# Optimization experiments

Measured on AMD Instinct MI355X. Metric: run time of the kernel, lower is better.

The kernel has to match this reference:

```python
import jax, jax.numpy as jnp
import numpy as np
from jax import lax

B, L, D, H = 48, 512, 384, 384


def setup_inputs() -> dict:
    key = jax.random.key(0)
    ks = jax.random.split(key, 8)
    def w(k, shape, fan):
        return jax.random.normal(k, shape, jnp.float32) / np.float32(np.sqrt(fan))
    return {
        "v": jax.random.normal(ks[0], (B, L, D), jnp.float32),
        "mask": jnp.ones((B, L), jnp.bool_),
        "Wp_cur": w(ks[1], (D, H), D),      # torch Wp (applied to v_i)
        "Wp_seq": w(ks[2], (D, H), D),      # torch Wp_ (applied to all of v)
        "V": w(ks[3], (H,), H),             # torch V: Linear(H, 1, bias=False)
        "W_ih": w(ks[4], (3 * H, 2 * D), 2 * D),  # GRUCell input weights
        "W_hh": w(ks[5], (3 * H, H), H),           # GRUCell hidden weights
        "b_ih": jnp.zeros((3 * H,), jnp.float32),
        "b_hh": jnp.zeros((3 * H,), jnp.float32),
    }


def _forward(v, mask, Wp_cur, Wp_seq, V, W_ih, W_hh, b_ih, b_hh):
    Bv, Lv, _ = v.shape
    Hh = W_hh.shape[1]
    # Torch recomputes Wp_(v) identically every step; hoist it (same math).
    Wpv = jnp.einsum('bld,dh->blh', v, Wp_seq)            # [B,L,H]
    neg = jnp.where(mask, 0.0, -1e30).astype(v.dtype)     # additive attention mask [B,L]

    def step(h, vi):                                       # vi: [B,D], h: [B,H]
        wpi = vi @ Wp_cur                                  # [B,H]
        x = jnp.tanh(Wpv + wpi[:, None, :])                # [B,L,H]
        s = jnp.einsum('blh,h->bl', x, V) + neg            # scores [B,L]
        a = jax.nn.softmax(s, axis=1)                      # masked softmax
        c = jnp.einsum('bl,bld->bd', a, v)                 # context [B,D]
        r = jnp.concatenate([vi, c], axis=1)               # [B,2D]
        gi = r @ W_ih.T + b_ih
        gh = h @ W_hh.T + b_hh
        ir, iz, inn = jnp.split(gi, 3, axis=1)
        hr, hz, hn = jnp.split(gh, 3, axis=1)
        rg = jax.nn.sigmoid(ir + hr)
        zg = jax.nn.sigmoid(iz + hz)
        ng = jnp.tanh(inn + rg * hn)
        hnew = (1.0 - zg) * ng + zg * h                    # PyTorch GRUCell update
        return hnew, hnew

    h0 = jnp.zeros((Bv, Hh), v.dtype)
    h_last, hs = lax.scan(jax.checkpoint(step), h0, jnp.swapaxes(v, 0, 1))
    hs = jnp.swapaxes(hs, 0, 1)                            # [B,L,H]
    # dropout p=0.0 -> identity; h = hs[:, -1]
    return hs, h_last


def reference(v, mask, Wp_cur, Wp_seq, V, W_ih, W_hh, b_ih, b_hh):
    return _forward(v, mask, Wp_cur, Wp_seq, V, W_ih, W_hh, b_ih, b_hh)
```

## Files before the change

### kernel.cpp

```cpp
#include <hip/hip_runtime.h>


typedef unsigned short u16;
typedef unsigned int u32;
typedef short short8 __attribute__((ext_vector_type(8)));
typedef float f32x4 __attribute__((ext_vector_type(4)));
typedef float f4 __attribute__((ext_vector_type(4)));
typedef _Float16 h2_t __attribute__((ext_vector_type(2)));
typedef _Float16 h8_t __attribute__((ext_vector_type(8)));

#define BDIM 48
#define LDIM 512
#define DDIM 384
#define HDIM 384

__device__ __forceinline__ float bf2f(u16 u) { return __uint_as_float(((u32)u) << 16); }
__device__ __forceinline__ u16 f2bf(float f) {
  u32 x = __float_as_uint(f);
  u32 r = (x + 0x7fffu + ((x >> 16) & 1u)) >> 16;
  return (u16)r;
}
__device__ __forceinline__ float sigm(float x) {
  return __builtin_amdgcn_rcpf(1.f + exp2f(-1.4426950408889634f * x));
}
__device__ __forceinline__ float tanh_f(float x) {
  float e = exp2f(2.885390081777927f * x);
  return 1.f - 2.f * __builtin_amdgcn_rcpf(e + 1.f);
}

__device__ __forceinline__ void load16(const void* src, long ld, int isf32,
                                       long row, int kbase, short8& o0, short8& o1)
{
  if (isf32) {
    const float* s = (const float*)src + row * ld + kbase;
    f4 q0 = *(const f4*)(s);
    f4 q1 = *(const f4*)(s + 4);
    f4 q2 = *(const f4*)(s + 8);
    f4 q3 = *(const f4*)(s + 12);
    short8 a, b;
    a[0] = (short)f2bf(q0[0]); a[1] = (short)f2bf(q0[1]);
    a[2] = (short)f2bf(q0[2]); a[3] = (short)f2bf(q0[3]);
    a[4] = (short)f2bf(q1[0]); a[5] = (short)f2bf(q1[1]);
    a[6] = (short)f2bf(q1[2]); a[7] = (short)f2bf(q1[3]);
    b[0] = (short)f2bf(q2[0]); b[1] = (short)f2bf(q2[1]);
    b[2] = (short)f2bf(q2[2]); b[3] = (short)f2bf(q2[3]);
    b[4] = (short)f2bf(q3[0]); b[5] = (short)f2bf(q3[1]);
    b[6] = (short)f2bf(q3[2]); b[7] = (short)f2bf(q3[3]);
    o0 = a; o1 = b;
  } else {
    const u16* s = (const u16*)src + row * ld + kbase;
    o0 = *(const short8*)s;
    o1 = *(const short8*)(s + 8);
  }
}

__global__ __launch_bounds__(256) void gemm_bt(
    const void* __restrict__ A1, const void* __restrict__ A2,
    long lda1, long lda2, int ksplit, int a1f, int a2f,
    const void* __restrict__ Bm, long ldb, int bfm,
    u16* __restrict__ Out, int N, int K,
    long strideA, long strideB, long strideO,
    const float* __restrict__ bias, int epi_exp2, int out_bf16)
{
  __shared__ u16 As[128][40];
  __shared__ u16 Bs[128][40];
  const int tid = threadIdx.x;
  const int lane = tid & 63;
  const int w = tid >> 6;
  const int wm = w >> 1, wn = w & 1;
  const int l15 = lane & 15, quad = lane >> 4;
  const long m0 = (long)blockIdx.x * 128;
  const long n0 = (long)blockIdx.y * 128;
  const int z = blockIdx.z;
  const char* A1p = (const char*)A1 + (long)z * strideA * (a1f ? 4 : 2);
  const char* A2p = (const char*)A2 + (long)z * strideA * (a2f ? 4 : 2);
  const char* Bp  = (const char*)Bm + (long)z * strideB * (bfm ? 4 : 2);
  u16* Op = Out + (long)z * strideO;

  const int r2 = tid & 127;
  const int half = tid >> 7;

  f32x4 acc[4][4];
#pragma unroll
  for (int a = 0; a < 4; a++)
#pragma unroll
    for (int c = 0; c < 4; c++) acc[a][c] = (f32x4){0.f, 0.f, 0.f, 0.f};

  for (int k0 = 0; k0 < K; k0 += 32) {
    const void* srcA; long lda; int kk; int af;
    if (k0 < ksplit) { srcA = A1p; lda = lda1; kk = k0; af = a1f; }
    else             { srcA = A2p; lda = lda2; kk = k0 - ksplit; af = a2f; }
    short8 a0, a1, b0, b1;
    load16(srcA, lda, af, m0 + r2, kk + half * 16, a0, a1);
    load16(Bp, ldb, bfm, n0 + r2, k0 + half * 16, b0, b1);
    __syncthreads();
    *(short8*)&As[r2][half * 16] = a0;
    *(short8*)&As[r2][half * 16 + 8] = a1;
    *(short8*)&Bs[r2][half * 16] = b0;
    *(short8*)&Bs[r2][half * 16 + 8] = b1;
    __syncthreads();
    short8 af_[4], bf_[4];
#pragma unroll
    for (int mt = 0; mt < 4; mt++) af_[mt] = *(const short8*)&As[wm * 64 + mt * 16 + l15][quad * 8];
#pragma unroll
    for (int nt = 0; nt < 4; nt++) bf_[nt] = *(const short8*)&Bs[wn * 64 + nt * 16 + l15][quad * 8];
#pragma unroll
    for (int mt = 0; mt < 4; mt++)
#pragma unroll
      for (int nt = 0; nt < 4; nt++)
        acc[mt][nt] = __builtin_amdgcn_mfma_f32_16x16x32_bf16(af_[mt], bf_[nt], acc[mt][nt], 0, 0, 0);
  }

#pragma unroll
  for (int mt = 0; mt < 4; mt++) {
#pragma unroll
    for (int nt = 0; nt < 4; nt++) {
      const long col = n0 + wn * 64 + nt * 16 + l15;
      float bv = bias ? bias[col] : 0.f;
#pragma unroll
      for (int rg = 0; rg < 4; rg++) {
        long row = m0 + wm * 64 + mt * 16 + quad * 4 + rg;
        float vv = acc[mt][nt][rg] + bv;
        if (epi_exp2) {
          float t = vv * 2.885390081777927f;
          t = fminf(fmaxf(t, -15.9f), 15.9f);
          vv = exp2f(t);
        }
        long idx = row * (long)N + col;
        if (out_bf16) Op[idx] = f2bf(vv);
        else ((_Float16*)Op)[idx] = (_Float16)vv;
      }
    }
  }
}

__global__ void transpose_f2b(const float* __restrict__ src, u16* __restrict__ dst,
                              int rows, int cols, long sstride, long dstride)
{
  __shared__ float t[32][33];
  const int bz = blockIdx.z;
  const float* s = src + (long)bz * sstride;
  u16* d = dst + (long)bz * dstride;
  const int c0 = blockIdx.x * 32, r0 = blockIdx.y * 32;
  const int tx = threadIdx.x, ty = threadIdx.y;
#pragma unroll
  for (int j = 0; j < 4; j++) t[ty + j * 8][tx] = s[(long)(r0 + ty + j * 8) * cols + c0 + tx];
  __syncthreads();
#pragma unroll
  for (int j = 0; j < 4; j++) d[(long)(c0 + ty + j * 8) * rows + r0 + tx] = f2bf(t[tx][ty + j * 8]);
}

__global__ __launch_bounds__(256) void attn_softmax(
    const _Float16* __restrict__ E, const _Float16* __restrict__ F,
    const float* __restrict__ Vw, u16* __restrict__ Aout)
{
  const int blk = blockIdx.x;
  const int x8 = blk & 7;
  const int rest = blk >> 3;
  const int i = rest & 511;
  const int b = x8 + 8 * (rest >> 9);
  const int tid = threadIdx.x;
  const int lane = tid & 63, w = tid >> 6;
  const int r = lane & 15, sub = lane >> 4;
  __shared__ float Tl[512];
  __shared__ float red[8];

  const h8_t* Fr = (const h8_t*)(F + ((long)b * LDIM + i) * HDIM + r * 24);
  h8_t fq0 = Fr[0], fq1 = Fr[1], fq2 = Fr[2];
  float fv[24], vv[24];
#pragma unroll
  for (int j = 0; j < 8; j++) {
    fv[j] = (float)fq0[j]; fv[8 + j] = (float)fq1[j]; fv[16 + j] = (float)fq2[j];
  }
  const float* Vp = Vw + r * 24;
#pragma unroll
  for (int j = 0; j < 24; j++) vv[j] = Vp[j];

  for (int li = 0; li < 32; ++li) {
    const int l = li * 16 + w * 4 + sub;
    const h8_t* Er = (const h8_t*)(E + ((long)b * LDIM + l) * HDIM + r * 24);
    h8_t e0 = Er[0], e1 = Er[1], e2 = Er[2];
    float p = 0.f;
#pragma unroll
    for (int j = 0; j < 8; j++) {
      p += vv[j]      * __builtin_amdgcn_rcpf((float)e0[j] * fv[j]      + 1.f);
      p += vv[8 + j]  * __builtin_amdgcn_rcpf((float)e1[j] * fv[8 + j]  + 1.f);
      p += vv[16 + j] * __builtin_amdgcn_rcpf((float)e2[j] * fv[16 + j] + 1.f);
    }
    p += __shfl_xor(p, 1);
    p += __shfl_xor(p, 2);
    p += __shfl_xor(p, 4);
    p += __shfl_xor(p, 8);
    if (r == 0) Tl[l] = p;
  }
  __syncthreads();

  const float t0 = Tl[tid], t1 = Tl[tid + 256];
  float mn = fminf(t0, t1);
#pragma unroll
  for (int off = 32; off; off >>= 1) mn = fminf(mn, __shfl_xor(mn, off));
  if (lane == 0) red[w] = mn;
  __syncthreads();
  const float mT = fminf(fminf(red[0], red[1]), fminf(red[2], red[3]));
  const float C2 = 2.885390081777927f;
  float p0 = exp2f(C2 * (mT - t0));
  float p1 = exp2f(C2 * (mT - t1));
  float ssum = p0 + p1;
#pragma unroll
  for (int off = 32; off; off >>= 1) ssum += __shfl_xor(ssum, off);
  if (lane == 0) red[4 + w] = ssum;
  __syncthreads();
  const float Z = (red[4] + red[5]) + (red[6] + red[7]);
  const float inv = __builtin_amdgcn_rcpf(Z);
  u16* Ar = Aout + ((long)b * LDIM + i) * LDIM;
  Ar[tid] = f2bf(p0 * inv);
  Ar[tid + 256] = f2bf(p1 * inv);
}

__global__ __launch_bounds__(512, 2) void recurrence(
    const float* __restrict__ Whh, const float* __restrict__ bhh_g,
    const _Float16* __restrict__ GI, u32* __restrict__ hslots,
    float* __restrict__ out)
{
  const int blk = blockIdx.x;
  const int x8 = blk & 7;
  const int s = blk >> 3;
  const int b = x8 + 8 * (s % 6);
  const int g = s / 6;
  const int tid = threadIdx.x;
  const int tx = tid & 15;
  const int ty = tid >> 4;

  __shared__ _Float16 hall[HDIM];
  __shared__ float gh[288];

  h2_t wv[9][12];
  float bh[9];
#pragma unroll
  for (int q = 0; q < 9; q++) {
    int rr = ty * 9 + q;
    int R = (rr / 96) * 384 + g * 96 + (rr % 96);
    const f4* wq = (const f4*)(Whh + (long)R * HDIM + tx * 24);
#pragma unroll
    for (int t6 = 0; t6 < 6; t6++) {
      f4 u = wq[t6];
      wv[q][2 * t6]     = (h2_t){(_Float16)u[0], (_Float16)u[1]};
      wv[q][2 * t6 + 1] = (h2_t){(_Float16)u[2], (_Float16)u[3]};
    }
    bh[q] = (tx == 0) ? bhh_g[R] : 0.f;
  }

  if (tid < HDIM) hall[tid] = (_Float16)0.f;
  __syncthreads();

  const long gi_base = (long)b * LDIM * 1152;
  const int own = tid >> 5;
  (void)own;
  float hprev = 0.f;

  for (int i = 0; i < LDIM; ++i) {
    float gir = 0.f, giz = 0.f, gin = 0.f;
    if (tid < 96) {
      const long gb = gi_base + (long)i * 1152 + g * 96 + tid;
      gir = (float)GI[gb];
      giz = (float)GI[gb + 384];
      gin = (float)GI[gb + 768];
    }

    if (i > 0) {
      if (tid < HDIM && (tid / 96) != g) {
        u32* p = hslots + (long)(i & 1) * (BDIM * HDIM) + (long)b * HDIM + tid;
        u32 val = __hip_atomic_load(p, __ATOMIC_RELAXED, __HIP_MEMORY_SCOPE_AGENT);
        while ((val >> 16) != (u32)i) {
          __builtin_amdgcn_s_sleep(1);
          val = __hip_atomic_load(p, __ATOMIC_RELAXED, __HIP_MEMORY_SCOPE_AGENT);
        }
        union { u16 u; _Float16 h; } cv;
        cv.u = (u16)val;
        hall[tid] = cv.h;
      }
      __syncthreads();
    }

    h2_t hv[12];
#pragma unroll
    for (int p = 0; p < 12; p++) hv[p] = *(const h2_t*)&hall[tx * 24 + 2 * p];
    float ac[9];
#pragma unroll
    for (int q = 0; q < 9; q++) {
      float a = 0.f;
#pragma unroll
      for (int p = 0; p < 12; p++) a = __builtin_amdgcn_fdot2(wv[q][p], hv[p], a, false);
      ac[q] = a;
    }
#pragma unroll
    for (int q = 0; q < 9; q++) {
      float a = ac[q];
      a += __shfl_xor(a, 1);
      a += __shfl_xor(a, 2);
      a += __shfl_xor(a, 4);
      a += __shfl_xor(a, 8);
      if (tx == 0) gh[ty * 9 + q] = a + bh[q];
    }
    __syncthreads();
    if (tid < 96) {
      const int j = g * 96 + tid;
      float hr = gh[tid], hz = gh[96 + tid], hn = gh[192 + tid];
      float rg = sigm(gir + hr);
      float zg = sigm(giz + hz);
      float ng = tanh_f(gin + rg * hn);
      float hnew = (1.f - zg) * ng + zg * hprev;
      hprev = hnew;
      out[((long)b * LDIM + i) * HDIM + j] = hnew;
      if (i == LDIM - 1) out[(long)BDIM * LDIM * HDIM + (long)b * HDIM + j] = hnew;
      union { _Float16 h; u16 u; } cv;
      cv.h = (_Float16)hnew;
      hall[j] = cv.h;
      if (i + 1 < LDIM) {
        u32 val = ((u32)(i + 1) << 16) | (u32)cv.u;
        __hip_atomic_store(
            hslots + (long)((i + 1) & 1) * (BDIM * HDIM) + (long)b * HDIM + j, val,
            __ATOMIC_RELAXED, __HIP_MEMORY_SCOPE_AGENT);
      }
    }
  }
}

extern "C" void kernel_launch(void* const* d_in, const int* in_sizes, int n_in,
                              void* d_out, int out_size, void* d_ws, size_t ws_size,
                              hipStream_t stream)
{
  (void)in_sizes; (void)n_in; (void)out_size; (void)ws_size;
  const float* v      = (const float*)d_in[0];
  const float* Wp_cur = (const float*)d_in[2];
  const float* Wp_seq = (const float*)d_in[3];
  const float* Vw     = (const float*)d_in[4];
  const float* W_ih   = (const float*)d_in[5];
  const float* W_hh   = (const float*)d_in[6];
  const float* b_ih   = (const float*)d_in[7];
  const float* b_hh   = (const float*)d_in[8];
  float* out = (float*)d_out;

  char* ws = (char*)d_ws;
  size_t off = 0;
  auto alloc = [&](size_t bytes) -> char* {
    char* p = ws + off;
    off += (bytes + 255) & ~(size_t)255;
    return p;
  };
  u32* hslots = (u32*)alloc((size_t)2 * 48 * 384 * 4);
  u16* WpSeqT = (u16*)alloc((size_t)384 * 384 * 2);
  u16* WpCurT = (u16*)alloc((size_t)384 * 384 * 2);
  u16* Cbuf   = (u16*)alloc((size_t)24576 * 384 * 2);
  u16* vT     = (u16*)alloc((size_t)48 * 384 * 512 * 2);
  char* region = alloc((size_t)24576 * 384 * 2 * 2 + (size_t)24576 * 512 * 2);
  _Float16* E  = (_Float16*)region;
  _Float16* F  = (_Float16*)(region + (size_t)24576 * 384 * 2);
  u16* Abuf    = (u16*)(region + (size_t)24576 * 384 * 2 * 2);
  _Float16* GI = (_Float16*)region;

  transpose_f2b<<<dim3(12, 12, 1), dim3(32, 8), 0, stream>>>(Wp_seq, WpSeqT, 384, 384, 0, 0);
  transpose_f2b<<<dim3(12, 12, 1), dim3(32, 8), 0, stream>>>(Wp_cur, WpCurT, 384, 384, 0, 0);
  transpose_f2b<<<dim3(12, 16, 48), dim3(32, 8), 0, stream>>>(v, vT, 512, 384,
                                                              (long)512 * 384, (long)384 * 512);

  gemm_bt<<<dim3(192, 3, 1), 256, 0, stream>>>(v, v, 384, 384, 1 << 30, 1, 1,
                                               WpSeqT, 384, 0,
                                               (u16*)E, 384, 384, 0, 0, 0, nullptr, 1, 0);
  gemm_bt<<<dim3(192, 3, 1), 256, 0, stream>>>(v, v, 384, 384, 1 << 30, 1, 1,
                                               WpCurT, 384, 0,
                                               (u16*)F, 384, 384, 0, 0, 0, nullptr, 1, 0);

  attn_softmax<<<dim3(24576), 256, 0, stream>>>(E, F, Vw, Abuf);

  gemm_bt<<<dim3(4, 3, 48), 256, 0, stream>>>(Abuf, Abuf, 512, 512, 1 << 30, 0, 0,
                                              vT, 512, 0,
                                              Cbuf, 384, 512,
                                              (long)512 * 512, (long)384 * 512, (long)512 * 384,
                                              nullptr, 0, 1);

  gemm_bt<<<dim3(192, 9, 1), 256, 0, stream>>>(v, Cbuf, 384, 384, 384, 1, 0,
                                               W_ih, 768, 1,
                                               (u16*)GI, 1152, 768, 0, 0, 0, b_ih, 0, 0);

  void* args[] = {(void*)&W_hh, (void*)&b_hh, (void*)&GI, (void*)&hslots, (void*)&out};
  hipLaunchCooperativeKernel(recurrence, dim3(192), dim3(512), args, 0, stream);
}
```

Measured before the change: 2.358 ms.

## Remove block barriers from GRU recurrence; poll tagged hidden state directly

Reworks the recurrence kernel so each 16-lane group owns three hidden units end-to-end. The group computes all three gate dot products, reduces them with shuffles, and applies the GRU update without shared memory or __syncthreads. Every thread now polls the full tagged hidden vector from global memory with vector loads. A fast-path buffer is written with workgroup scope and read with sc0 loads, and a mirror buffer written with agent scope serves as a fallback after many spins. GI values for the next step are prefetched one iteration ahead. The cost targeted is barrier and LDS round-trip latency per step; the risk is that the workgroup-scope fast path may not be coherent across CUs, so it could spin until the fallback kicks in, and every thread now generates global polling traffic.

```diff
diff --git a/kernel.cpp b/kernel.cpp
--- a/kernel.cpp
+++ b/kernel.cpp
@@ -8,6 +8,7 @@
 typedef float f4 __attribute__((ext_vector_type(4)));
 typedef _Float16 h2_t __attribute__((ext_vector_type(2)));
 typedef _Float16 h8_t __attribute__((ext_vector_type(8)));
+typedef u32 u32x4 __attribute__((ext_vector_type(4)));
 
 #define BDIM 48
 #define LDIM 512
@@ -219,8 +220,8 @@
 
 __global__ __launch_bounds__(512, 2) void recurrence(
     const float* __restrict__ Whh, const float* __restrict__ bhh_g,
-    const _Float16* __restrict__ GI, u32* __restrict__ hslots,
-    float* __restrict__ out)
+    const _Float16* __restrict__ GI, u32* __restrict__ hfast,
+    u32* __restrict__ hmir, float* __restrict__ out)
 {
   const int blk = blockIdx.x;
   const int x8 = blk & 7;
@@ -230,16 +231,13 @@
   const int tid = threadIdx.x;
   const int tx = tid & 15;
   const int ty = tid >> 4;
-
-  __shared__ _Float16 hall[HDIM];
-  __shared__ float gh[288];
+  const int jbase = g * 96 + ty * 3;
 
   h2_t wv[9][12];
   float bh[9];
 #pragma unroll
   for (int q = 0; q < 9; q++) {
-    int rr = ty * 9 + q;
-    int R = (rr / 96) * 384 + g * 96 + (rr % 96);
+    const int R = (q % 3) * 384 + jbase + (q / 3);
     const f4* wq = (const f4*)(Whh + (long)R * HDIM + tx * 24);
 #pragma unroll
     for (int t6 = 0; t6 < 6; t6++) {
@@ -247,80 +245,148 @@
       wv[q][2 * t6]     = (h2_t){(_Float16)u[0], (_Float16)u[1]};
       wv[q][2 * t6 + 1] = (h2_t){(_Float16)u[2], (_Float16)u[3]};
     }
-    bh[q] = (tx == 0) ? bhh_g[R] : 0.f;
-  }
-
-  if (tid < HDIM) hall[tid] = (_Float16)0.f;
-  __syncthreads();
-
-  const long gi_base = (long)b * LDIM * 1152;
-  const int own = tid >> 5;
-  (void)own;
-  float hprev = 0.f;
+    bh[q] = bhh_g[R];
+  }
+
+  float gc[9], gn[9];
+#pragma unroll
+  for (int q = 0; q < 9; q++) gn[q] = 0.f;
+  if (tx == 0) {
+    const _Float16* gp = GI + (long)b * LDIM * 1152 + jbase;
+#pragma unroll
+    for (int q = 0; q < 9; q++) gn[q] = (float)gp[(q % 3) * 384 + (q / 3)];
+  }
+
+  const u32* fb = hfast + (long)b * HDIM + tx * 24;
+  const u32* mb = hmir  + (long)b * HDIM + tx * 24;
+  u32* sf = hfast + (long)b * HDIM + jbase;
+  u32* sm = hmir  + (long)b * HDIM + jbase;
+  const int SLOT = BDIM * HDIM;
+
+  float hp0 = 0.f, hp1 = 0.f, hp2 = 0.f;
+  int mode = 0;
 
   for (int i = 0; i < LDIM; ++i) {
-    float gir = 0.f, giz = 0.f, gin = 0.f;
-    if (tid < 96) {
-      const long gb = gi_base + (long)i * 1152 + g * 96 + tid;
-      gir = (float)GI[gb];
-      giz = (float)GI[gb + 384];
-      gin = (float)GI[gb + 768];
-    }
-
-    if (i > 0) {
-      if (tid < HDIM && (tid / 96) != g) {
-        u32* p = hslots + (long)(i & 1) * (BDIM * HDIM) + (long)b * HDIM + tid;
-        u32 val = __hip_atomic_load(p, __ATOMIC_RELAXED, __HIP_MEMORY_SCOPE_AGENT);
-        while ((val >> 16) != (u32)i) {
-          __builtin_amdgcn_s_sleep(1);
-          val = __hip_atomic_load(p, __ATOMIC_RELAXED, __HIP_MEMORY_SCOPE_AGENT);
+#pragma unroll
+    for (int q = 0; q < 9; q++) gc[q] = gn[q];
+
+    h2_t hv[12];
+    const bool hh = (i > 0);
+    if (hh) {
+      const u32 itag = (u32)i << 16;
+      const int ofs = (i & 1) ? SLOT : 0;
+      const u32* fp = fb + ofs;
+      const u32* mp = mb + ofs;
+      u32x4 q0, q1, q2, q3, q4, q5;
+      int spins = 0;
+      for (;;) {
+        if (mode == 0) {
+          asm volatile(
+              "global_load_dwordx4 %0, %6, off sc0\n\t"
+              "global_load_dwordx4 %1, %6, off offset:16 sc0\n\t"
+              "global_load_dwordx4 %2, %6, off offset:32 sc0\n\t"
+              "global_load_dwordx4 %3, %6, off offset:48 sc0\n\t"
+              "global_load_dwordx4 %4, %6, off offset:64 sc0\n\t"
+              "global_load_dwordx4 %5, %6, off offset:80 sc0"
+              : "=v"(q0), "=v"(q1), "=v"(q2), "=v"(q3), "=v"(q4), "=v"(q5)
+              : "v"(fp));
+        } else {
+          asm volatile(
+              "global_load_dwordx4 %0, %6, off sc0 sc1\n\t"
+              "global_load_dwordx4 %1, %6, off offset:16 sc0 sc1\n\t"
+              "global_load_dwordx4 %2, %6, off offset:32 sc0 sc1\n\t"
+              "global_load_dwordx4 %3, %6, off offset:48 sc0 sc1\n\t"
+              "global_load_dwordx4 %4, %6, off offset:64 sc0 sc1\n\t"
+              "global_load_dwordx4 %5, %6, off offset:80 sc0 sc1"
+              : "=v"(q0), "=v"(q1), "=v"(q2), "=v"(q3), "=v"(q4), "=v"(q5)
+              : "v"(mp));
         }
-        union { u16 u; _Float16 h; } cv;
-        cv.u = (u16)val;
-        hall[tid] = cv.h;
-      }
-      __syncthreads();
-    }
-
-    h2_t hv[12];
-#pragma unroll
-    for (int p = 0; p < 12; p++) hv[p] = *(const h2_t*)&hall[tx * 24 + 2 * p];
+        asm volatile("s_waitcnt vmcnt(0)" ::: "memory");
+        __builtin_amdgcn_sched_barrier(0);
+        u32 bad = 0;
+#pragma unroll
+        for (int k = 0; k < 4; k++) {
+          bad |= q0[k] ^ itag; bad |= q1[k] ^ itag; bad |= q2[k] ^ itag;
+          bad |= q3[k] ^ itag; bad |= q4[k] ^ itag; bad |= q5[k] ^ itag;
+        }
+        if (!(bad >> 16)) break;
+        if (++spins > 200) mode = 1;
+        __builtin_amdgcn_s_sleep(1);
+      }
+#define UNPK(QQ, P0)                                                        \
+      {                                                                     \
+        union { u32 u; h2_t h; } c0_, c1_;                                  \
+        c0_.u = (QQ[0] & 0xffffu) | (QQ[1] << 16);                          \
+        c1_.u = (QQ[2] & 0xffffu) | (QQ[3] << 16);                          \
+        hv[P0] = c0_.h; hv[P0 + 1] = c1_.h;                                 \
+      }
+      UNPK(q0, 0) UNPK(q1, 2) UNPK(q2, 4) UNPK(q3, 6) UNPK(q4, 8) UNPK(q5, 10)
+#undef UNPK
+    }
+
+    if (tx == 0 && i + 1 < LDIM) {
+      const _Float16* gp = GI + ((long)b * LDIM + (i + 1)) * 1152 + jbase;
+#pragma unroll
+      for (int q = 0; q < 9; q++) gn[q] = (float)gp[(q % 3) * 384 + (q / 3)];
+    }
+
     float ac[9];
-#pragma unroll
-    for (int q = 0; q < 9; q++) {
-      float a = 0.f;
-#pragma unroll
-      for (int p = 0; p < 12; p++) a = __builtin_amdgcn_fdot2(wv[q][p], hv[p], a, false);
-      ac[q] = a;
-    }
-#pragma unroll
-    for (int q = 0; q < 9; q++) {
-      float a = ac[q];
-      a += __shfl_xor(a, 1);
-      a += __shfl_xor(a, 2);
-      a += __shfl_xor(a, 4);
-      a += __shfl_xor(a, 8);
-      if (tx == 0) gh[ty * 9 + q] = a + bh[q];
-    }
-    __syncthreads();
-    if (tid < 96) {
-      const int j = g * 96 + tid;
-      float hr = gh[tid], hz = gh[96 + tid], hn = gh[192 + tid];
-      float rg = sigm(gir + hr);
-      float zg = sigm(giz + hz);
-      float ng = tanh_f(gin + rg * hn);
-      float hnew = (1.f - zg) * ng + zg * hprev;
-      hprev = hnew;
-      out[((long)b * LDIM + i) * HDIM + j] = hnew;
-      if (i == LDIM - 1) out[(long)BDIM * LDIM * HDIM + (long)b * HDIM + j] = hnew;
-      union { _Float16 h; u16 u; } cv;
-      cv.h = (_Float16)hnew;
-      hall[j] = cv.h;
+    if (hh) {
+#pragma unroll
+      for (int q = 0; q < 9; q++) {
+        float a = 0.f;
+#pragma unroll
+        for (int p = 0; p < 12; p++) a = __builtin_amdgcn_fdot2(wv[q][p], hv[p], a, false);
+        a += __shfl_xor(a, 1);
+        a += __shfl_xor(a, 2);
+        a += __shfl_xor(a, 4);
+        a += __shfl_xor(a, 8);
+        ac[q] = a;
+      }
+    } else {
+#pragma unroll
+      for (int q = 0; q < 9; q++) ac[q] = 0.f;
+    }
+
+    if (tx == 0) {
+      float h0n, h1n, h2n;
+      {
+        float rg = sigm(gc[0] + ac[0] + bh[0]);
+        float zg = sigm(gc[1] + ac[1] + bh[1]);
+        float ng = tanh_f(gc[2] + rg * (ac[2] + bh[2]));
+        h0n = (1.f - zg) * ng + zg * hp0;
+      }
+      {
+        float rg = sigm(gc[3] + ac[3] + bh[3]);
+        float zg = sigm(gc[4] + ac[4] + bh[4]);
+        float ng = tanh_f(gc[5] + rg * (ac[5] + bh[5]));
+        h1n = (1.f - zg) * ng + zg * hp1;
+      }
+      {
+        float rg = sigm(gc[6] + ac[6] + bh[6]);
+        float zg = sigm(gc[7] + ac[7] + bh[7]);
+        float ng = tanh_f(gc[8] + rg * (ac[8] + bh[8]));
+        h2n = (1.f - zg) * ng + zg * hp2;
+      }
+      hp0 = h0n; hp1 = h1n; hp2 = h2n;
+      const long orow = ((long)b * LDIM + i) * HDIM + jbase;
+      out[orow] = h0n; out[orow + 1] = h1n; out[orow + 2] = h2n;
+      if (i == LDIM - 1) {
+        const long fo = (long)BDIM * LDIM * HDIM + (long)b * HDIM + jbase;
+        out[fo] = h0n; out[fo + 1] = h1n; out[fo + 2] = h2n;
+      }
       if (i + 1 < LDIM) {
-        u32 val = ((u32)(i + 1) << 16) | (u32)cv.u;
-        __hip_atomic_store(
-            hslots + (long)((i + 1) & 1) * (BDIM * HDIM) + (long)b * HDIM + j, val,
-            __ATOMIC_RELAXED, __HIP_MEMORY_SCOPE_AGENT);
+        const int wofs = ((i + 1) & 1) ? SLOT : 0;
+        const u32 t = (u32)(i + 1) << 16;
+        union { _Float16 h; u16 u; } c0, c1, c2;
+        c0.h = (_Float16)h0n; c1.h = (_Float16)h1n; c2.h = (_Float16)h2n;
+        const u32 v0 = t | (u32)c0.u, v1 = t | (u32)c1.u, v2 = t | (u32)c2.u;
+        __hip_atomic_store(sf + wofs + 0, v0, __ATOMIC_RELAXED, __HIP_MEMORY_SCOPE_WORKGROUP);
+        __hip_atomic_store(sf + wofs + 1, v1, __ATOMIC_RELAXED, __HIP_MEMORY_SCOPE_WORKGROUP);
+        __hip_atomic_store(sf + wofs + 2, v2, __ATOMIC_RELAXED, __HIP_MEMORY_SCOPE_WORKGROUP);
+        __hip_atomic_store(sm + wofs + 0, v0, __ATOMIC_RELAXED, __HIP_MEMORY_SCOPE_AGENT);
+        __hip_atomic_store(sm + wofs + 1, v1, __ATOMIC_RELAXED, __HIP_MEMORY_SCOPE_AGENT);
+        __hip_atomic_store(sm + wofs + 2, v2, __ATOMIC_RELAXED, __HIP_MEMORY_SCOPE_AGENT);
       }
     }
   }
@@ -348,7 +414,8 @@
     off += (bytes + 255) & ~(size_t)255;
     return p;
   };
-  u32* hslots = (u32*)alloc((size_t)2 * 48 * 384 * 4);
+  u32* hfast  = (u32*)alloc((size_t)2 * 48 * 384 * 4);
+  u32* hmir   = (u32*)alloc((size_t)2 * 48 * 384 * 4);
   u16* WpSeqT = (u16*)alloc((size_t)384 * 384 * 2);
   u16* WpCurT = (u16*)alloc((size_t)384 * 384 * 2);
   u16* Cbuf   = (u16*)alloc((size_t)24576 * 384 * 2);
@@ -383,6 +450,7 @@
                                                W_ih, 768, 1,
                                                (u16*)GI, 1152, 768, 0, 0, 0, b_ih, 0, 0);
 
-  void* args[] = {(void*)&W_hh, (void*)&b_hh, (void*)&GI, (void*)&hslots, (void*)&out};
+  void* args[] = {(void*)&W_hh, (void*)&b_hh, (void*)&GI, (void*)&hfast,
+                  (void*)&hmir, (void*)&out};
   hipLaunchCooperativeKernel(recurrence, dim3(192), dim3(512), args, 0, stream);
 }
```

Result: slower. 7.129 ms (+202.3%).
